# Performance work log

Hardware: AMD Instinct MI355X
Metric: run time of the kernel (lower is better)

Reference implementation:

```python
import jax, jax.numpy as jnp
import numpy as np

B, T, F, H = 256, 512, 64, 512


def setup_inputs() -> dict:
    key = jax.random.key(0)
    ks = jax.random.split(key, 7)
    s_ih = 1.0 / np.sqrt(H)
    return {
        "x": jax.random.normal(ks[0], (B, T, F), dtype=jnp.float32),
        # PyTorch nn.GRU layout: rows ordered [reset; update; new], each (H, in)
        "W_ih": jax.random.uniform(ks[1], (3 * H, F), minval=-s_ih, maxval=s_ih, dtype=jnp.float32),
        "W_hh": jax.random.uniform(ks[2], (3 * H, H), minval=-s_ih, maxval=s_ih, dtype=jnp.float32),
        "b_ih": jax.random.uniform(ks[3], (3 * H,), minval=-s_ih, maxval=s_ih, dtype=jnp.float32),
        "b_hh": jax.random.uniform(ks[4], (3 * H,), minval=-s_ih, maxval=s_ih, dtype=jnp.float32),
        "head_w": jax.random.uniform(ks[5], (1, H), minval=-s_ih, maxval=s_ih, dtype=jnp.float32),
        "head_b": jax.random.uniform(ks[6], (1,), minval=-s_ih, maxval=s_ih, dtype=jnp.float32),
    }


def _gru_last_hidden(x, W_ih, W_hh, b_ih, b_hh):
    # Precompute input projections for all timesteps: (B, T, 3H)
    gi_all = jnp.einsum("btf,gf->btg", x, W_ih) + b_ih
    gi_all = jnp.swapaxes(gi_all, 0, 1)  # (T, B, 3H) for scan

    def step(h, gi):
        gh = h @ W_hh.T + b_hh  # (B, 3H)
        i_r, i_z, i_n = jnp.split(gi, 3, axis=-1)
        h_r, h_z, h_n = jnp.split(gh, 3, axis=-1)
        r = jax.nn.sigmoid(i_r + h_r)
        z = jax.nn.sigmoid(i_z + h_z)
        n = jnp.tanh(i_n + r * h_n)
        h_new = (1.0 - z) * n + z * h
        return h_new, None

    h0 = jnp.zeros((x.shape[0], W_hh.shape[1]), dtype=x.dtype)
    h_last, _ = jax.lax.scan(step, h0, gi_all)
    return h_last  # (B, H)


def reference(x, W_ih, W_hh, b_ih, b_hh, head_w, head_b):
    last = _gru_last_hidden(x, W_ih, W_hh, b_ih, b_hh)  # out[:, -1, :]
    # head_dropout is identity in eval mode
    y = last @ head_w.T + head_b  # (B, 1)
    return y.squeeze(-1)  # (B,)
```

## Files before the change

kernel.cpp:

```cpp
#include <hip/hip_runtime.h>
#include <hip/hip_bf16.h>

typedef __attribute__((ext_vector_type(4))) float f32x4;
typedef __attribute__((ext_vector_type(8))) short s16x8;
typedef __attribute__((ext_vector_type(4))) unsigned short u16x4;

#define DEVFN static __device__ __forceinline__

constexpr int B_ = 256, T_ = 512, F_ = 64, H_ = 512;
constexpr int NB = 16;
constexpr int NS = 8;
constexpr int MT = B_ / NB;
constexpr int NT = H_ / NS;
constexpr int NGRID = NB * NS;
constexpr int NTHR = 256;

DEVFN unsigned short f2bf(float f) {
  unsigned int u = __builtin_bit_cast(unsigned int, f);
  u += 0x7fffu + ((u >> 16) & 1u);
  return (unsigned short)(u >> 16);
}

DEVFN float sigmoidf_(float x) { return 1.f / (1.f + __expf(-x)); }
DEVFN float tanhf_(float x) {
  float a = fabsf(x);
  float t = __expf(-2.f * a);
  float r = (1.f - t) / (1.f + t);
  return x < 0.f ? -r : r;
}

__global__ __launch_bounds__(NTHR, 1)
void gru_scan(const float* __restrict__ x, const float* __restrict__ Wih,
              const float* __restrict__ Whh, const float* __restrict__ bih,
              const float* __restrict__ bhh, const float* __restrict__ hw,
              const float* __restrict__ hb, float* __restrict__ out,
              unsigned short* __restrict__ Hbuf, int* __restrict__ flagbase)
{
  const int tid = threadIdx.x;
  const int lane = tid & 63;
  const int wv = tid >> 6;
  const int gi = (int)blockIdx.x & (NB - 1);
  const int sj = (int)blockIdx.x >> 4;

  __shared__ __align__(16) unsigned char h_lds[MT * H_ * 2];
  __shared__ __align__(16) unsigned char x_lds[MT * F_ * 2];

  int* gflags = flagbase + gi * 16;

  const int frow = lane & 15;
  const int g8 = (lane >> 4) * 8;
  const int g16 = (lane >> 4) * 16;
  const int gc = sj * NT + wv * 16 + frow;

  s16x8 whh_f[3][16];
  s16x8 wih_f[3][2];
#pragma unroll
  for (int g = 0; g < 3; ++g) {
    const float* wr = Whh + ((size_t)(g * H_ + gc)) * H_;
#pragma unroll
    for (int kk = 0; kk < 16; ++kk) {
      const float4 p0 = *(const float4*)(wr + kk * 32 + g8);
      const float4 p1 = *(const float4*)(wr + kk * 32 + g8 + 4);
      s16x8 f;
      f[0] = (short)f2bf(p0.x); f[1] = (short)f2bf(p0.y);
      f[2] = (short)f2bf(p0.z); f[3] = (short)f2bf(p0.w);
      f[4] = (short)f2bf(p1.x); f[5] = (short)f2bf(p1.y);
      f[6] = (short)f2bf(p1.z); f[7] = (short)f2bf(p1.w);
      whh_f[g][kk] = f;
    }
    const float* wr2 = Wih + ((size_t)(g * H_ + gc)) * F_;
#pragma unroll
    for (int k2 = 0; k2 < 2; ++k2) {
      const float4 p0 = *(const float4*)(wr2 + k2 * 32 + g8);
      const float4 p1 = *(const float4*)(wr2 + k2 * 32 + g8 + 4);
      s16x8 f;
      f[0] = (short)f2bf(p0.x); f[1] = (short)f2bf(p0.y);
      f[2] = (short)f2bf(p0.z); f[3] = (short)f2bf(p0.w);
      f[4] = (short)f2bf(p1.x); f[5] = (short)f2bf(p1.y);
      f[6] = (short)f2bf(p1.z); f[7] = (short)f2bf(p1.w);
      wih_f[g][k2] = f;
    }
  }

  const float b_r  = bih[gc] + bhh[gc];
  const float b_z  = bih[H_ + gc] + bhh[H_ + gc];
  const float b_in = bih[2 * H_ + gc];
  const float b_hn = bhh[2 * H_ + gc];
  const float hw_l = hw[gc];

  const int aswz = (frow & 7) << 4;
  char* hrow_ptr = (char*)h_lds + frow * 1024;
  char* xrow_ptr = (char*)x_lds + frow * 128;

  float hstate[4] = {0.f, 0.f, 0.f, 0.f};

  for (int t = 0; t < T_; ++t) {
    {
      const int m = tid >> 4, fs = tid & 15;
      const float4 xv =
          *(const float4*)(x + (((size_t)(gi * MT + m)) * T_ + t) * F_ + fs * 4);
      u16x4 xb;
      xb[0] = f2bf(xv.x); xb[1] = f2bf(xv.y);
      xb[2] = f2bf(xv.z); xb[3] = f2bf(xv.w);
      *(u16x4*)((char*)x_lds + m * 128 + ((fs * 8) ^ ((m & 7) << 4))) = xb;
    }
    if (t > 0) {
      {
        int f = 0x7fffffff;
        for (;;) {
          if (lane < NS)
            f = __hip_atomic_load(&gflags[lane], __ATOMIC_RELAXED,
                                  __HIP_MEMORY_SCOPE_AGENT);
          if (__all(f >= t)) break;
          __builtin_amdgcn_s_sleep(2);
        }
      }
      const unsigned long long* hsrc =
          (const unsigned long long*)(Hbuf + ((size_t)(t & 1) * B_ + gi * MT) * H_);
#pragma unroll
      for (int q = 0; q < 8; ++q) {
        const int idx = tid + q * 256;
        unsigned long long v = __hip_atomic_load(
            (unsigned long long*)(hsrc + idx), __ATOMIC_RELAXED,
            __HIP_MEMORY_SCOPE_AGENT);
        const int m = idx >> 7;
        const int cb = (idx & 127) * 8;
        *(unsigned long long*)((char*)h_lds + m * 1024 + (cb ^ ((m & 7) << 4))) = v;
      }
    }
    __syncthreads();

    f32x4 ar = {0.f, 0.f, 0.f, 0.f}, az = {0.f, 0.f, 0.f, 0.f};
    f32x4 anx = {0.f, 0.f, 0.f, 0.f}, anh = {0.f, 0.f, 0.f, 0.f};
#pragma unroll
    for (int k2 = 0; k2 < 2; ++k2) {
      const s16x8 a = *(const s16x8*)(xrow_ptr + ((k2 * 64 + g16) ^ aswz));
      ar  = __builtin_amdgcn_mfma_f32_16x16x32_bf16(a, wih_f[0][k2], ar, 0, 0, 0);
      az  = __builtin_amdgcn_mfma_f32_16x16x32_bf16(a, wih_f[1][k2], az, 0, 0, 0);
      anx = __builtin_amdgcn_mfma_f32_16x16x32_bf16(a, wih_f[2][k2], anx, 0, 0, 0);
    }
    if (t > 0) {
#pragma unroll
      for (int kk = 0; kk < 16; ++kk) {
        const s16x8 a = *(const s16x8*)(hrow_ptr + ((kk * 64 + g16) ^ aswz));
        ar  = __builtin_amdgcn_mfma_f32_16x16x32_bf16(a, whh_f[0][kk], ar, 0, 0, 0);
        az  = __builtin_amdgcn_mfma_f32_16x16x32_bf16(a, whh_f[1][kk], az, 0, 0, 0);
        anh = __builtin_amdgcn_mfma_f32_16x16x32_bf16(a, whh_f[2][kk], anh, 0, 0, 0);
      }
    }

#pragma unroll
    for (int e = 0; e < 4; ++e) {
      const float rr = sigmoidf_(ar[e] + b_r);
      const float zz = sigmoidf_(az[e] + b_z);
      const float nn = tanhf_(anx[e] + b_in + rr * (anh[e] + b_hn));
      hstate[e] = (1.f - zz) * nn + zz * hstate[e];
    }

    if (t < T_ - 1) {
      unsigned short hbf[4];
#pragma unroll
      for (int e = 0; e < 4; ++e) hbf[e] = f2bf(hstate[e]);
#pragma unroll
      for (int e = 0; e < 4; ++e) {
        const unsigned int other = (unsigned int)__shfl_xor((int)hbf[e], 1);
        if (!(lane & 1)) {
          const int m = ((lane >> 4) << 2) + e;
          const unsigned int pack = (unsigned int)hbf[e] | (other << 16);
          unsigned int* dst = (unsigned int*)(Hbuf +
              (((size_t)((t + 1) & 1) * B_) + gi * MT + m) * H_ + gc);
          __hip_atomic_store(dst, pack, __ATOMIC_RELAXED,
                             __HIP_MEMORY_SCOPE_AGENT);
        }
      }
      __syncthreads();
      if (tid == 0)
        __hip_atomic_store(&gflags[sj], t + 1, __ATOMIC_RELAXED,
                           __HIP_MEMORY_SCOPE_AGENT);
    }
  }

  {
    float part[4];
#pragma unroll
    for (int e = 0; e < 4; ++e) part[e] = hstate[e] * hw_l;
#pragma unroll
    for (int mask = 1; mask < 16; mask <<= 1) {
#pragma unroll
      for (int e = 0; e < 4; ++e) part[e] += __shfl_xor(part[e], mask);
    }
    if ((lane & 15) == 0) {
      const float addb = (sj == 0 && wv == 0) ? hb[0] : 0.f;
#pragma unroll
      for (int e = 0; e < 4; ++e)
        atomicAdd(out + gi * MT + ((lane >> 4) << 2) + e, part[e] + addb);
    }
  }
}

extern "C" void kernel_launch(void* const* d_in, const int* in_sizes, int n_in,
                              void* d_out, int out_size, void* d_ws, size_t ws_size,
                              hipStream_t stream)
{
  const float* x   = (const float*)d_in[0];
  const float* Wih = (const float*)d_in[1];
  const float* Whh = (const float*)d_in[2];
  const float* bih = (const float*)d_in[3];
  const float* bhh = (const float*)d_in[4];
  const float* hw  = (const float*)d_in[5];
  const float* hb  = (const float*)d_in[6];
  float* out = (float*)d_out;
  unsigned short* Hbuf = (unsigned short*)d_ws;
  int* flags = (int*)((char*)d_ws + (size_t)2 * B_ * H_ * 2);

  hipMemsetAsync(d_out, 0, (size_t)out_size * sizeof(float), stream);
  hipMemsetAsync(flags, 0, (size_t)NB * 16 * sizeof(int), stream);

  gru_scan<<<dim3(NGRID), dim3(NTHR), 0, stream>>>(
      x, Wih, Whh, bih, bhh, hw, hb, out, Hbuf, flags);
}
```

Measured before the change: 2.238 ms.

## Replace per-step flag barrier with timestep-tagged hidden-state words

Each exchanged bf16 pair of the hidden state is now stored as a 64-bit word with the timestep in the upper half. Consumers poll the data itself until every tag matches the current step, so the separate flag array, its memset and the block-wide barrier before the flag store are gone. LDS buffers for h and x are double-buffered by step parity, which removes the hazard that the removed barrier used to guard. In exchange, each step moves twice as many bytes through global memory, and correctness relies on tag comparison against stale or uninitialized workspace.

```diff
diff --git a/kernel.cpp b/kernel.cpp
--- a/kernel.cpp
+++ b/kernel.cpp
@@ -4,6 +4,8 @@
 typedef __attribute__((ext_vector_type(4))) float f32x4;
 typedef __attribute__((ext_vector_type(8))) short s16x8;
 typedef __attribute__((ext_vector_type(4))) unsigned short u16x4;
+typedef unsigned long long u64;
+typedef unsigned int u32;
 
 #define DEVFN static __device__ __forceinline__
 
@@ -14,9 +16,10 @@
 constexpr int NT = H_ / NS;
 constexpr int NGRID = NB * NS;
 constexpr int NTHR = 256;
+constexpr int C2 = H_ / 2;
 
 DEVFN unsigned short f2bf(float f) {
-  unsigned int u = __builtin_bit_cast(unsigned int, f);
+  u32 u = __builtin_bit_cast(u32, f);
   u += 0x7fffu + ((u >> 16) & 1u);
   return (unsigned short)(u >> 16);
 }
@@ -34,7 +37,7 @@
               const float* __restrict__ Whh, const float* __restrict__ bih,
               const float* __restrict__ bhh, const float* __restrict__ hw,
               const float* __restrict__ hb, float* __restrict__ out,
-              unsigned short* __restrict__ Hbuf, int* __restrict__ flagbase)
+              u64* __restrict__ Hpk)
 {
   const int tid = threadIdx.x;
   const int lane = tid & 63;
@@ -42,10 +45,8 @@
   const int gi = (int)blockIdx.x & (NB - 1);
   const int sj = (int)blockIdx.x >> 4;
 
-  __shared__ __align__(16) unsigned char h_lds[MT * H_ * 2];
-  __shared__ __align__(16) unsigned char x_lds[MT * F_ * 2];
-
-  int* gflags = flagbase + gi * 16;
+  __shared__ __align__(16) unsigned char h_lds[2][MT * 1024];
+  __shared__ __align__(16) unsigned char x_lds[2][MT * 128];
 
   const int frow = lane & 15;
   const int g8 = (lane >> 4) * 8;
@@ -89,12 +90,36 @@
   const float hw_l = hw[gc];
 
   const int aswz = (frow & 7) << 4;
-  char* hrow_ptr = (char*)h_lds + frow * 1024;
-  char* xrow_ptr = (char*)x_lds + frow * 128;
+  const int c2own = sj * 32 + wv * 8 + (frow >> 1);
 
   float hstate[4] = {0.f, 0.f, 0.f, 0.f};
 
   for (int t = 0; t < T_; ++t) {
+    const int p = t & 1;
+    if (t > 0) {
+      const u64* src = Hpk + ((size_t)p * B_ + gi * MT) * C2 + tid;
+      u64 pk[16];
+#pragma unroll
+      for (int q = 0; q < 16; ++q)
+        pk[q] = __hip_atomic_load(src + q * C2, __ATOMIC_RELAXED,
+                                  __HIP_MEMORY_SCOPE_AGENT);
+      for (;;) {
+        bool bad = false;
+#pragma unroll
+        for (int q = 0; q < 16; ++q) bad |= ((u32)(pk[q] >> 32) != (u32)t);
+        if (!__any(bad)) break;
+        __builtin_amdgcn_s_sleep(1);
+#pragma unroll
+        for (int q = 0; q < 16; ++q)
+          if ((u32)(pk[q] >> 32) != (u32)t)
+            pk[q] = __hip_atomic_load(src + q * C2, __ATOMIC_RELAXED,
+                                      __HIP_MEMORY_SCOPE_AGENT);
+      }
+#pragma unroll
+      for (int q = 0; q < 16; ++q)
+        *(u32*)(&h_lds[p][q * 1024 + ((tid * 4) ^ ((q & 7) << 4))]) =
+            (u32)pk[q];
+    }
     {
       const int m = tid >> 4, fs = tid & 15;
       const float4 xv =
@@ -102,34 +127,12 @@
       u16x4 xb;
       xb[0] = f2bf(xv.x); xb[1] = f2bf(xv.y);
       xb[2] = f2bf(xv.z); xb[3] = f2bf(xv.w);
-      *(u16x4*)((char*)x_lds + m * 128 + ((fs * 8) ^ ((m & 7) << 4))) = xb;
-    }
-    if (t > 0) {
-      {
-        int f = 0x7fffffff;
-        for (;;) {
-          if (lane < NS)
-            f = __hip_atomic_load(&gflags[lane], __ATOMIC_RELAXED,
-                                  __HIP_MEMORY_SCOPE_AGENT);
-          if (__all(f >= t)) break;
-          __builtin_amdgcn_s_sleep(2);
-        }
-      }
-      const unsigned long long* hsrc =
-          (const unsigned long long*)(Hbuf + ((size_t)(t & 1) * B_ + gi * MT) * H_);
-#pragma unroll
-      for (int q = 0; q < 8; ++q) {
-        const int idx = tid + q * 256;
-        unsigned long long v = __hip_atomic_load(
-            (unsigned long long*)(hsrc + idx), __ATOMIC_RELAXED,
-            __HIP_MEMORY_SCOPE_AGENT);
-        const int m = idx >> 7;
-        const int cb = (idx & 127) * 8;
-        *(unsigned long long*)((char*)h_lds + m * 1024 + (cb ^ ((m & 7) << 4))) = v;
-      }
+      *(u16x4*)(&x_lds[p][m * 128 + ((fs * 8) ^ ((m & 7) << 4))]) = xb;
     }
     __syncthreads();
 
+    const char* xrow_ptr = (const char*)&x_lds[p][frow * 128];
+    const char* hrow_ptr = (const char*)&h_lds[p][frow * 1024];
     f32x4 ar = {0.f, 0.f, 0.f, 0.f}, az = {0.f, 0.f, 0.f, 0.f};
     f32x4 anx = {0.f, 0.f, 0.f, 0.f}, anh = {0.f, 0.f, 0.f, 0.f};
 #pragma unroll
@@ -161,22 +164,18 @@
       unsigned short hbf[4];
 #pragma unroll
       for (int e = 0; e < 4; ++e) hbf[e] = f2bf(hstate[e]);
+      u64* dstbase = Hpk + ((size_t)((t + 1) & 1) * B_ + gi * MT) * C2;
 #pragma unroll
       for (int e = 0; e < 4; ++e) {
-        const unsigned int other = (unsigned int)__shfl_xor((int)hbf[e], 1);
+        const u32 other = (u32)__shfl_xor((int)hbf[e], 1);
         if (!(lane & 1)) {
           const int m = ((lane >> 4) << 2) + e;
-          const unsigned int pack = (unsigned int)hbf[e] | (other << 16);
-          unsigned int* dst = (unsigned int*)(Hbuf +
-              (((size_t)((t + 1) & 1) * B_) + gi * MT + m) * H_ + gc);
-          __hip_atomic_store(dst, pack, __ATOMIC_RELAXED,
+          const u64 val = ((u64)(u32)(t + 1) << 32) |
+                          (u64)((u32)hbf[e] | (other << 16));
+          __hip_atomic_store(dstbase + m * C2 + c2own, val, __ATOMIC_RELAXED,
                              __HIP_MEMORY_SCOPE_AGENT);
         }
       }
-      __syncthreads();
-      if (tid == 0)
-        __hip_atomic_store(&gflags[sj], t + 1, __ATOMIC_RELAXED,
-                           __HIP_MEMORY_SCOPE_AGENT);
     }
   }
 
@@ -210,12 +209,10 @@
   const float* hw  = (const float*)d_in[5];
   const float* hb  = (const float*)d_in[6];
   float* out = (float*)d_out;
-  unsigned short* Hbuf = (unsigned short*)d_ws;
-  int* flags = (int*)((char*)d_ws + (size_t)2 * B_ * H_ * 2);
+  u64* Hpk = (u64*)d_ws;
 
   hipMemsetAsync(d_out, 0, (size_t)out_size * sizeof(float), stream);
-  hipMemsetAsync(flags, 0, (size_t)NB * 16 * sizeof(int), stream);
 
   gru_scan<<<dim3(NGRID), dim3(NTHR), 0, stream>>>(
-      x, Wih, Whh, bih, bhh, hw, hb, out, Hbuf, flags);
-}
+      x, Wih, Whh, bih, bhh, hw, hb, out, Hpk);
+}
```

Result: faster. 1.933 ms (-13.6%).
